# Kernel tuning notes

Hardware: AMD Instinct MI355X
Metric: run time of the kernel (lower is better)

## Reference

```python
import jax, jax.numpy as jnp
import numpy as np
import math

H = 12  # heads (init kwarg)
KEEP_RATE = 0.7  # forward arg keep_rate (< 1 -> token pruning path)


def setup_inputs() -> dict:
    key = jax.random.key(0)
    k0, k1, k2 = jax.random.split(key, 3)
    b, n, c = 32, 577, 768  # ViT-B/16 @ 384px: 576 patches + CLS
    x = jax.random.normal(k0, (b, n, c), dtype=jnp.float32)
    # nn.Linear(dim, dim*3) and nn.Linear(dim, dim); kaiming-ish scale
    W_qkv = jax.random.normal(k1, (c, 3 * c), dtype=jnp.float32) / np.sqrt(c).astype(np.float32)
    b_qkv = jnp.zeros((3 * c,), dtype=jnp.float32)
    W_out = jax.random.normal(k2, (c, c), dtype=jnp.float32) / np.sqrt(c).astype(np.float32)
    b_out = jnp.zeros((c,), dtype=jnp.float32)
    return {"x": x, "keep_rate": KEEP_RATE, "W_qkv": W_qkv, "b_qkv": b_qkv,
            "W_out": W_out, "b_out": b_out}


def reference(x, keep_rate, W_qkv, b_qkv, W_out, b_out):
    b, n, c = x.shape
    d = c // H
    scale = (c / H) ** -0.5
    # qkv projection + split into heads: 'b n (h d) -> b h n d'
    qkv = x @ W_qkv + b_qkv                      # [b, n, 3c]
    q, k, v = jnp.split(qkv, 3, axis=-1)
    split_heads = lambda t: t.reshape(b, n, H, d).transpose(0, 2, 1, 3)
    q, k, v = split_heads(q), split_heads(k), split_heads(v)
    dots = jnp.einsum('bhid,bhjd->bhij', q, k) * scale   # [b,h,n,n]
    attention = jax.nn.softmax(dots, axis=-1)
    out = jnp.einsum('bhij,bhjd->bhid', attention, v)    # [b,h,n,d]
    out = out.transpose(0, 2, 1, 3).reshape(b, n, c)     # 'b h n d -> b n (h d)'
    out = out @ W_out + b_out                            # to_out (dropout=0)
    final_tokens = n - 1
    if keep_rate < 1:
        final_tokens = math.ceil(keep_rate * final_tokens)
        # CLS-token attention to patch tokens, averaged over heads
        class_attention = attention[:, :, 0, 1:].mean(axis=1)   # [b, n-1]
        _, ind = jax.lax.top_k(class_attention, final_tokens)    # [b, final_tokens]
        ind = jnp.sort(ind, axis=1)
        index = jnp.broadcast_to(ind[:, :, None], (b, final_tokens, c))
        return (x, index, ind, class_attention, final_tokens)
    return (out, None, None, None, final_tokens)
```

## Files before the change

### kernel.cpp

```cpp
#include <hip/hip_runtime.h>
#include <hip/hip_bf16.h>
#include <math.h>

#define BATCH 32
#define NTOK 577
#define NPATCH 576
#define CDIM 768
#define HEADS 12
#define DHEAD 64
#define W3 2304
#define FT 404

#define WS_WTIL  24576
#define WS_DBIAS 319488
#define WS_DOTS  319872
#define WS_IND   541440

#define O_X      0ULL
#define O_INDEX  14180352ULL
#define O_IND    24109056ULL
#define O_CA     24121984ULL
#define O_FT     24140416ULL

__global__ __launch_bounds__(256) void k_fold(const float* __restrict__ x,
                                              const float* __restrict__ W,
                                              const float* __restrict__ bias,
                                              float* __restrict__ wtil,
                                              float* __restrict__ dbias) {
    __shared__ float x0s[CDIM];
    __shared__ float red[256];
    __shared__ float qs[DHEAD];
    const int b = blockIdx.x, h = blockIdx.y, tid = threadIdx.x;
    for (int i = tid; i < CDIM; i += 256) x0s[i] = x[(size_t)b * NTOK * CDIM + i];
    __syncthreads();
    {
        const int d = tid & 63, seg = tid >> 6;
        const float* Wq = W + (size_t)(h * DHEAD + d);
        float acc = 0.f;
        const int c0 = seg * 192;
        #pragma unroll 8
        for (int c = c0; c < c0 + 192; c++)
            acc += x0s[c] * Wq[(size_t)c * W3];
        red[tid] = acc;
    }
    __syncthreads();
    if (tid < DHEAD) {
        float q = red[tid] + red[tid + 64] + red[tid + 128] + red[tid + 192]
                + bias[h * DHEAD + tid];
        qs[tid] = q;
        float t = q * bias[CDIM + h * DHEAD + tid];
        #pragma unroll
        for (int off = 32; off; off >>= 1) t += __shfl_down(t, off);
        if (tid == 0) dbias[b * HEADS + h] = t;
    }
    __syncthreads();
    for (int c = tid; c < CDIM; c += 256) {
        const float* wr = W + (size_t)c * W3 + CDIM + h * DHEAD;
        float acc = 0.f;
        #pragma unroll
        for (int d = 0; d < DHEAD; d += 4) {
            float4 a = *reinterpret_cast<const float4*>(wr + d);
            acc += a.x * qs[d] + a.y * qs[d + 1] + a.z * qs[d + 2] + a.w * qs[d + 3];
        }
        wtil[((size_t)b * HEADS + h) * CDIM + c] = acc;
    }
}

__global__ __launch_bounds__(256) void k_dots(const float* __restrict__ x,
                                              const float* __restrict__ wtil,
                                              const float* __restrict__ dbias,
                                              float* __restrict__ dots,
                                              float* __restrict__ out0) {
    __shared__ float wt[HEADS * CDIM];
    __shared__ float db[HEADS];
    const int b = blockIdx.x, tid = threadIdx.x;
    for (int i = tid; i < HEADS * CDIM; i += 256) wt[i] = wtil[(size_t)b * HEADS * CDIM + i];
    if (tid < HEADS) db[tid] = dbias[b * HEADS + tid];
    __syncthreads();
    const int wave = tid >> 6, lane = tid & 63;
    for (int it = 0; it < 8; it++) {
        const int j = blockIdx.y * 32 + it * 4 + wave;
        if (j >= NTOK) break;
        const float4* xp = reinterpret_cast<const float4*>(x + ((size_t)b * NTOK + j) * CDIM);
        float4* op = reinterpret_cast<float4*>(out0 + ((size_t)b * NTOK + j) * CDIM);
        float acc[HEADS];
        #pragma unroll
        for (int h = 0; h < HEADS; h++) acc[h] = 0.f;
        #pragma unroll
        for (int i = 0; i < 3; i++) {
            float4 a = xp[i * 64 + lane];
            op[i * 64 + lane] = a;
            const int cbase = i * 256 + lane * 4;
            #pragma unroll
            for (int h = 0; h < HEADS; h++) {
                float4 w = *reinterpret_cast<const float4*>(&wt[h * CDIM + cbase]);
                acc[h] += a.x * w.x + a.y * w.y + a.z * w.z + a.w * w.w;
            }
        }
        #pragma unroll
        for (int off = 32; off; off >>= 1)
            #pragma unroll
            for (int h = 0; h < HEADS; h++) acc[h] += __shfl_xor(acc[h], off);
        if (lane == 0) {
            #pragma unroll
            for (int h = 0; h < HEADS; h++)
                dots[((size_t)b * HEADS + h) * NTOK + j] = 0.125f * (acc[h] + db[h]);
        }
    }
}

__global__ __launch_bounds__(768) void k_catopk(const float* __restrict__ dots,
                                                float* __restrict__ ca_out,
                                                float* __restrict__ ind_out,
                                                float* __restrict__ ft_out,
                                                int* __restrict__ ind_ws,
                                                int write_ft) {
    __shared__ float dl[HEADS * NTOK];
    __shared__ float mh[HEADS], sh[HEADS];
    __shared__ unsigned int vals[NPATCH];
    __shared__ int flags[NPATCH];
    const int b = blockIdx.x, tid = threadIdx.x;
    for (int i = tid; i < HEADS * NTOK; i += 768) dl[i] = dots[(size_t)b * HEADS * NTOK + i];
    __syncthreads();
    {
        const int w = tid >> 6, lane = tid & 63;
        const float* row = dl + w * NTOK;
        float m = -3.4e38f;
        for (int j = lane; j < NTOK; j += 64) m = fmaxf(m, row[j]);
        #pragma unroll
        for (int off = 32; off; off >>= 1) m = fmaxf(m, __shfl_xor(m, off));
        float s = 0.f;
        for (int j = lane; j < NTOK; j += 64) s += expf(row[j] - m);
        #pragma unroll
        for (int off = 32; off; off >>= 1) s += __shfl_xor(s, off);
        if (lane == 0) { mh[w] = m; sh[w] = s; }
    }
    __syncthreads();
    if (tid < NPATCH) {
        float ca = 0.f;
        #pragma unroll
        for (int h = 0; h < HEADS; h++)
            ca += expf(dl[h * NTOK + 1 + tid] - mh[h]) / sh[h];
        ca *= (1.f / 12.f);
        ca_out[(size_t)b * NPATCH + tid] = ca;
        vals[tid] = __float_as_uint(ca);
    }
    __syncthreads();
    if (tid < NPATCH) {
        const unsigned int myv = vals[tid];
        int rank = 0;
        for (int j = 0; j < NPATCH; j++) {
            const unsigned int v = vals[j];
            rank += (v > myv) || (v == myv && j < tid);
        }
        flags[tid] = (rank < FT) ? 1 : 0;
    }
    __syncthreads();
    if (tid < NPATCH && flags[tid]) {
        int pos = 0;
        for (int j = 0; j < tid; j++) pos += flags[j];
        ind_ws[b * FT + pos] = tid;
        ind_out[(size_t)b * FT + pos] = (float)tid;
    }
    if (b == 0 && tid == 0 && write_ft) ft_out[0] = (float)FT;
}

__global__ __launch_bounds__(256) void k_bcast(const int* __restrict__ ind,
                                               float* __restrict__ out1) {
    const unsigned int g = blockIdx.x * 256u + threadIdx.x;
    const unsigned int e = g * 4u;
    const unsigned int row = e / CDIM;
    const float v = (float)ind[row];
    float4 o; o.x = v; o.y = v; o.z = v; o.w = v;
    *reinterpret_cast<float4*>(out1 + e) = o;
}

extern "C" void kernel_launch(void* const* d_in, const int* in_sizes, int n_in,
                              void* d_out, int out_size, void* d_ws, size_t ws_size,
                              hipStream_t stream) {
    const float* x  = (const float*)d_in[0];
    const float* W  = (const float*)d_in[2];
    const float* bq = (const float*)d_in[3];
    float* ws = (float*)d_ws;
    float* out = (float*)d_out;

    k_fold<<<dim3(BATCH, HEADS), 256, 0, stream>>>(x, W, bq, ws + WS_WTIL, ws + WS_DBIAS);
    k_dots<<<dim3(BATCH, 19), 256, 0, stream>>>(x, ws + WS_WTIL, ws + WS_DBIAS, ws + WS_DOTS, out + O_X);
    const int write_ft = (out_size > (int)O_FT) ? 1 : 0;
    k_catopk<<<BATCH, 768, 0, stream>>>(ws + WS_DOTS, out + O_CA, out + O_IND, out + O_FT,
                                        (int*)(ws + WS_IND), write_ft);
    k_bcast<<<9696, 256, 0, stream>>>((const int*)(ws + WS_IND), out + O_INDEX);
}
```

Measured before the change: 227.1 us.

## Fuse four kernels into one persistent kernel with global flag synchronization

Merges the fold, dots, class-attention/top-k and broadcast kernels into one launch over a (batch, 19) grid. Stages are ordered per batch with release/acquire flags stored in the not-yet-written index output buffer, which is later overwritten. This removes three kernel launches and their inter-kernel gaps. In exchange it risks deadlock or timeouts if the 608 blocks are not all co-resident, serializes the top-k step on one block per batch, and depends on sentinel values in the output buffer, so a leftover sentinel from a previous call could let a wait pass early.

```diff
diff --git a/kernel.cpp b/kernel.cpp
--- a/kernel.cpp
+++ b/kernel.cpp
@@ -1,5 +1,4 @@
 #include <hip/hip_runtime.h>
-#include <hip/hip_bf16.h>
 #include <math.h>
 
 #define BATCH 32
@@ -10,6 +9,7 @@
 #define DHEAD 64
 #define W3 2304
 #define FT 404
+#define JBLK 19
 
 #define WS_WTIL  24576
 #define WS_DBIAS 319488
@@ -22,157 +22,213 @@
 #define O_CA     24121984ULL
 #define O_FT     24140416ULL
 
-__global__ __launch_bounds__(256) void k_fold(const float* __restrict__ x,
-                                              const float* __restrict__ W,
-                                              const float* __restrict__ bias,
-                                              float* __restrict__ wtil,
-                                              float* __restrict__ dbias) {
-    __shared__ float x0s[CDIM];
-    __shared__ float red[256];
-    __shared__ float qs[DHEAD];
-    const int b = blockIdx.x, h = blockIdx.y, tid = threadIdx.x;
-    for (int i = tid; i < CDIM; i += 256) x0s[i] = x[(size_t)b * NTOK * CDIM + i];
+#define SENT 0x5EE7F1A6u
+#define SPIN_GUARD (1 << 18)
+
+__device__ __forceinline__ unsigned flag_ld_acq(const unsigned* p) {
+    return __hip_atomic_load(p, __ATOMIC_ACQUIRE, __HIP_MEMORY_SCOPE_AGENT);
+}
+__device__ __forceinline__ void flag_st_rel(unsigned* p, unsigned v) {
+    __hip_atomic_store(p, v, __ATOMIC_RELEASE, __HIP_MEMORY_SCOPE_AGENT);
+}
+__device__ __forceinline__ void wait_flags(const unsigned* base, int n, int stride) {
+    for (int i = 0; i < n; ++i) {
+        const unsigned* p = base + (size_t)i * (size_t)stride;
+        int guard = 0;
+        while (flag_ld_acq(p) != SENT) {
+            __builtin_amdgcn_s_sleep(16);
+            if (++guard > SPIN_GUARD) break;
+        }
+    }
+}
+
+__global__ __launch_bounds__(256, 3) void k_mega(
+        const float* __restrict__ x, const float* __restrict__ W,
+        const float* __restrict__ bq, float* __restrict__ ws,
+        float* out, int write_ft)
+{
+    __shared__ float smem[HEADS * CDIM];
+    __shared__ float db[HEADS];
+    __shared__ float mh[HEADS], sh[HEADS];
+    __shared__ unsigned vals[NPATCH];
+    __shared__ int flags[NPATCH];
+
+    const int b = blockIdx.x, y = blockIdx.y, tid = threadIdx.x;
+    float* const wtil  = ws + WS_WTIL;
+    float* const dbias = ws + WS_DBIAS;
+    float* const dots  = ws + WS_DOTS;
+    int*   const indws = (int*)(ws + WS_IND);
+    unsigned* const idxU = (unsigned*)(out + O_INDEX);
+    #define FCELL(row, c) (idxU + (((size_t)b * FT + (size_t)(row)) * CDIM + (c)))
+
+    if (y < HEADS) {
+        const int h = y;
+        float* const x0s = smem;
+        float* const red = smem + CDIM;
+        float* const qs  = smem + CDIM + 256;
+        if (tid < CDIM / 4)
+            ((float4*)x0s)[tid] = ((const float4*)(x + (size_t)b * NTOK * CDIM))[tid];
+        __syncthreads();
+        {
+            const int d = tid & 63, seg = tid >> 6;
+            const float* Wq = W + (size_t)(h * DHEAD + d);
+            float acc = 0.f;
+            const int c0 = seg * 192;
+            #pragma unroll 8
+            for (int c = c0; c < c0 + 192; c++)
+                acc += x0s[c] * Wq[(size_t)c * W3];
+            red[tid] = acc;
+        }
+        __syncthreads();
+        if (tid < DHEAD) {
+            float q = red[tid] + red[tid + 64] + red[tid + 128] + red[tid + 192]
+                    + bq[h * DHEAD + tid];
+            qs[tid] = q;
+            float t = q * bq[CDIM + h * DHEAD + tid];
+            #pragma unroll
+            for (int off = 32; off; off >>= 1) t += __shfl_down(t, off);
+            if (tid == 0) dbias[b * HEADS + h] = t;
+        }
+        __syncthreads();
+        for (int c = tid; c < CDIM; c += 256) {
+            const float* wr = W + (size_t)c * W3 + CDIM + h * DHEAD;
+            float acc = 0.f;
+            #pragma unroll
+            for (int d = 0; d < DHEAD; d += 4) {
+                float4 a = *reinterpret_cast<const float4*>(wr + d);
+                acc += a.x * qs[d] + a.y * qs[d + 1] + a.z * qs[d + 2] + a.w * qs[d + 3];
+            }
+            wtil[((size_t)b * HEADS + h) * CDIM + c] = acc;
+        }
+        __syncthreads();
+        if (tid == 0) { __threadfence(); flag_st_rel(FCELL(h, 2), SENT); }
+    }
+
+    if (tid == 0) wait_flags(FCELL(0, 2), HEADS, CDIM);
     __syncthreads();
+
     {
-        const int d = tid & 63, seg = tid >> 6;
-        const float* Wq = W + (size_t)(h * DHEAD + d);
-        float acc = 0.f;
-        const int c0 = seg * 192;
-        #pragma unroll 8
-        for (int c = c0; c < c0 + 192; c++)
-            acc += x0s[c] * Wq[(size_t)c * W3];
-        red[tid] = acc;
-    }
-    __syncthreads();
-    if (tid < DHEAD) {
-        float q = red[tid] + red[tid + 64] + red[tid + 128] + red[tid + 192]
-                + bias[h * DHEAD + tid];
-        qs[tid] = q;
-        float t = q * bias[CDIM + h * DHEAD + tid];
-        #pragma unroll
-        for (int off = 32; off; off >>= 1) t += __shfl_down(t, off);
-        if (tid == 0) dbias[b * HEADS + h] = t;
-    }
-    __syncthreads();
-    for (int c = tid; c < CDIM; c += 256) {
-        const float* wr = W + (size_t)c * W3 + CDIM + h * DHEAD;
-        float acc = 0.f;
-        #pragma unroll
-        for (int d = 0; d < DHEAD; d += 4) {
-            float4 a = *reinterpret_cast<const float4*>(wr + d);
-            acc += a.x * qs[d] + a.y * qs[d + 1] + a.z * qs[d + 2] + a.w * qs[d + 3];
-        }
-        wtil[((size_t)b * HEADS + h) * CDIM + c] = acc;
-    }
-}
-
-__global__ __launch_bounds__(256) void k_dots(const float* __restrict__ x,
-                                              const float* __restrict__ wtil,
-                                              const float* __restrict__ dbias,
-                                              float* __restrict__ dots,
-                                              float* __restrict__ out0) {
-    __shared__ float wt[HEADS * CDIM];
-    __shared__ float db[HEADS];
-    const int b = blockIdx.x, tid = threadIdx.x;
-    for (int i = tid; i < HEADS * CDIM; i += 256) wt[i] = wtil[(size_t)b * HEADS * CDIM + i];
-    if (tid < HEADS) db[tid] = dbias[b * HEADS + tid];
-    __syncthreads();
-    const int wave = tid >> 6, lane = tid & 63;
-    for (int it = 0; it < 8; it++) {
-        const int j = blockIdx.y * 32 + it * 4 + wave;
-        if (j >= NTOK) break;
-        const float4* xp = reinterpret_cast<const float4*>(x + ((size_t)b * NTOK + j) * CDIM);
-        float4* op = reinterpret_cast<float4*>(out0 + ((size_t)b * NTOK + j) * CDIM);
-        float acc[HEADS];
-        #pragma unroll
-        for (int h = 0; h < HEADS; h++) acc[h] = 0.f;
-        #pragma unroll
-        for (int i = 0; i < 3; i++) {
-            float4 a = xp[i * 64 + lane];
-            op[i * 64 + lane] = a;
-            const int cbase = i * 256 + lane * 4;
-            #pragma unroll
-            for (int h = 0; h < HEADS; h++) {
-                float4 w = *reinterpret_cast<const float4*>(&wt[h * CDIM + cbase]);
-                acc[h] += a.x * w.x + a.y * w.y + a.z * w.z + a.w * w.w;
-            }
-        }
-        #pragma unroll
-        for (int off = 32; off; off >>= 1)
-            #pragma unroll
-            for (int h = 0; h < HEADS; h++) acc[h] += __shfl_xor(acc[h], off);
-        if (lane == 0) {
+        float* const wt = smem;
+        {
+            const float4* s4 = (const float4*)(wtil + (size_t)b * HEADS * CDIM);
+            float4* d4 = (float4*)wt;
+            for (int i = tid; i < HEADS * CDIM / 4; i += 256) d4[i] = s4[i];
+        }
+        if (tid < HEADS) db[tid] = dbias[b * HEADS + tid];
+        __syncthreads();
+        const int wave = tid >> 6, lane = tid & 63;
+        for (int it = 0; it < 8; it++) {
+            const int j = y * 32 + it * 4 + wave;
+            if (j >= NTOK) break;
+            const float4* xp = (const float4*)(x + ((size_t)b * NTOK + j) * CDIM);
+            float4* op = (float4*)(out + O_X + ((size_t)b * NTOK + j) * CDIM);
+            float acc[HEADS];
+            #pragma unroll
+            for (int h = 0; h < HEADS; h++) acc[h] = 0.f;
+            #pragma unroll
+            for (int i = 0; i < 3; i++) {
+                float4 a = xp[i * 64 + lane];
+                op[i * 64 + lane] = a;
+                const int cbase = i * 256 + lane * 4;
+                #pragma unroll
+                for (int h = 0; h < HEADS; h++) {
+                    float4 w = *(const float4*)(&wt[h * CDIM + cbase]);
+                    acc[h] += a.x * w.x + a.y * w.y + a.z * w.z + a.w * w.w;
+                }
+            }
+            #pragma unroll
+            for (int off = 32; off; off >>= 1)
+                #pragma unroll
+                for (int h = 0; h < HEADS; h++) acc[h] += __shfl_xor(acc[h], off);
+            if (lane == 0) {
+                #pragma unroll
+                for (int h = 0; h < HEADS; h++)
+                    dots[((size_t)b * HEADS + h) * NTOK + j] = 0.125f * (acc[h] + db[h]);
+            }
+        }
+        __syncthreads();
+        if (tid == 0) { __threadfence(); flag_st_rel(FCELL(y, 1), SENT); }
+    }
+
+    if (y == 0) {
+        if (tid == 0) wait_flags(FCELL(0, 1), JBLK, CDIM);
+        __syncthreads();
+        float* const dl = smem;
+        {
+            const float4* s4 = (const float4*)(dots + (size_t)b * HEADS * NTOK);
+            float4* d4 = (float4*)dl;
+            for (int i = tid; i < HEADS * NTOK / 4; i += 256) d4[i] = s4[i];
+        }
+        __syncthreads();
+        {
+            const int w = tid >> 6, lane = tid & 63;
+            #pragma unroll
+            for (int hh = 0; hh < 3; hh++) {
+                const int h = w * 3 + hh;
+                const float* row = dl + h * NTOK;
+                float m = -3.4e38f;
+                for (int j = lane; j < NTOK; j += 64) m = fmaxf(m, row[j]);
+                #pragma unroll
+                for (int off = 32; off; off >>= 1) m = fmaxf(m, __shfl_xor(m, off));
+                float s = 0.f;
+                for (int j = lane; j < NTOK; j += 64) s += expf(row[j] - m);
+                #pragma unroll
+                for (int off = 32; off; off >>= 1) s += __shfl_xor(s, off);
+                if (lane == 0) { mh[h] = m; sh[h] = s; }
+            }
+        }
+        __syncthreads();
+        for (int t = tid; t < NPATCH; t += 256) {
+            float ca = 0.f;
             #pragma unroll
             for (int h = 0; h < HEADS; h++)
-                dots[((size_t)b * HEADS + h) * NTOK + j] = 0.125f * (acc[h] + db[h]);
-        }
-    }
-}
-
-__global__ __launch_bounds__(768) void k_catopk(const float* __restrict__ dots,
-                                                float* __restrict__ ca_out,
-                                                float* __restrict__ ind_out,
-                                                float* __restrict__ ft_out,
-                                                int* __restrict__ ind_ws,
-                                                int write_ft) {
-    __shared__ float dl[HEADS * NTOK];
-    __shared__ float mh[HEADS], sh[HEADS];
-    __shared__ unsigned int vals[NPATCH];
-    __shared__ int flags[NPATCH];
-    const int b = blockIdx.x, tid = threadIdx.x;
-    for (int i = tid; i < HEADS * NTOK; i += 768) dl[i] = dots[(size_t)b * HEADS * NTOK + i];
-    __syncthreads();
+                ca += expf(dl[h * NTOK + 1 + t] - mh[h]) / sh[h];
+            ca *= (1.f / 12.f);
+            out[O_CA + (size_t)b * NPATCH + t] = ca;
+            vals[t] = __float_as_uint(ca);
+        }
+        __syncthreads();
+        for (int t = tid; t < NPATCH; t += 256) {
+            const unsigned myv = vals[t];
+            int rank = 0;
+            for (int j = 0; j < NPATCH; j++) {
+                const unsigned v = vals[j];
+                rank += (v > myv) || (v == myv && j < t);
+            }
+            flags[t] = (rank < FT) ? 1 : 0;
+        }
+        __syncthreads();
+        for (int t = tid; t < NPATCH; t += 256) {
+            if (flags[t]) {
+                int pos = 0;
+                for (int j = 0; j < t; j++) pos += flags[j];
+                indws[b * FT + pos] = t;
+                out[O_IND + (size_t)b * FT + pos] = (float)t;
+            }
+        }
+        if (b == 0 && tid == 0 && write_ft) out[O_FT] = (float)FT;
+        __syncthreads();
+        if (tid == 0) {
+            __threadfence();
+            for (int i = 0; i < JBLK; i++) flag_st_rel(FCELL(i, 0), SENT);
+        }
+    } else {
+        if (tid == 0) wait_flags(FCELL(y, 0), 1, 0);
+        __syncthreads();
+    }
+
     {
-        const int w = tid >> 6, lane = tid & 63;
-        const float* row = dl + w * NTOK;
-        float m = -3.4e38f;
-        for (int j = lane; j < NTOK; j += 64) m = fmaxf(m, row[j]);
-        #pragma unroll
-        for (int off = 32; off; off >>= 1) m = fmaxf(m, __shfl_xor(m, off));
-        float s = 0.f;
-        for (int j = lane; j < NTOK; j += 64) s += expf(row[j] - m);
-        #pragma unroll
-        for (int off = 32; off; off >>= 1) s += __shfl_xor(s, off);
-        if (lane == 0) { mh[w] = m; sh[w] = s; }
-    }
-    __syncthreads();
-    if (tid < NPATCH) {
-        float ca = 0.f;
-        #pragma unroll
-        for (int h = 0; h < HEADS; h++)
-            ca += expf(dl[h * NTOK + 1 + tid] - mh[h]) / sh[h];
-        ca *= (1.f / 12.f);
-        ca_out[(size_t)b * NPATCH + tid] = ca;
-        vals[tid] = __float_as_uint(ca);
-    }
-    __syncthreads();
-    if (tid < NPATCH) {
-        const unsigned int myv = vals[tid];
-        int rank = 0;
-        for (int j = 0; j < NPATCH; j++) {
-            const unsigned int v = vals[j];
-            rank += (v > myv) || (v == myv && j < tid);
-        }
-        flags[tid] = (rank < FT) ? 1 : 0;
-    }
-    __syncthreads();
-    if (tid < NPATCH && flags[tid]) {
-        int pos = 0;
-        for (int j = 0; j < tid; j++) pos += flags[j];
-        ind_ws[b * FT + pos] = tid;
-        ind_out[(size_t)b * FT + pos] = (float)tid;
-    }
-    if (b == 0 && tid == 0 && write_ft) ft_out[0] = (float)FT;
-}
-
-__global__ __launch_bounds__(256) void k_bcast(const int* __restrict__ ind,
-                                               float* __restrict__ out1) {
-    const unsigned int g = blockIdx.x * 256u + threadIdx.x;
-    const unsigned int e = g * 4u;
-    const unsigned int row = e / CDIM;
-    const float v = (float)ind[row];
-    float4 o; o.x = v; o.y = v; o.z = v; o.w = v;
-    *reinterpret_cast<float4*>(out1 + e) = o;
+        const int K = (FT - 1 - y) / JBLK + 1;
+        const int total = K * 192;
+        for (int f = tid; f < total; f += 256) {
+            const int k = f / 192, c = f - k * 192;
+            const int t = y + k * JBLK;
+            const float v = (float)indws[b * FT + t];
+            float4 o; o.x = v; o.y = v; o.z = v; o.w = v;
+            ((float4*)(out + O_INDEX + ((size_t)b * FT + t) * CDIM))[c] = o;
+        }
+    }
+    #undef FCELL
 }
 
 extern "C" void kernel_launch(void* const* d_in, const int* in_sizes, int n_in,
@@ -183,11 +239,6 @@
     const float* bq = (const float*)d_in[3];
     float* ws = (float*)d_ws;
     float* out = (float*)d_out;
-
-    k_fold<<<dim3(BATCH, HEADS), 256, 0, stream>>>(x, W, bq, ws + WS_WTIL, ws + WS_DBIAS);
-    k_dots<<<dim3(BATCH, 19), 256, 0, stream>>>(x, ws + WS_WTIL, ws + WS_DBIAS, ws + WS_DOTS, out + O_X);
     const int write_ft = (out_size > (int)O_FT) ? 1 : 0;
-    k_catopk<<<BATCH, 768, 0, stream>>>(ws + WS_DOTS, out + O_CA, out + O_IND, out + O_FT,
-                                        (int*)(ws + WS_IND), write_ft);
-    k_bcast<<<9696, 256, 0, stream>>>((const int*)(ws + WS_IND), out + O_INDEX);
-}
+    k_mega<<<dim3(BATCH, JBLK), 256, 0, stream>>>(x, W, bq, ws, out, write_ft);
+}
```

New measurement: 615.2 us. 2.71x slower.

## Fuse top-k with index broadcast and batch four samples per fold block

Applied to the files above, without the earlier changes.

The fold kernel now handles four batch items per block, so each W_q/W_k column read is shared across four samples, and its grid shrinks to 96 blocks. The class-attention/top-k kernel is merged with the index broadcast kernel, which removes one launch and the workspace index round trip. Selected positions are compacted with ballot and popcount prefix sums instead of serial per-thread scans. The fused kernel is replicated across 8 y-blocks that each recompute softmax and ranks redundantly to split the broadcast writes, which adds duplicated compute in exchange.

```diff
diff --git a/kernel.cpp b/kernel.cpp
--- a/kernel.cpp
+++ b/kernel.cpp
@@ -1,5 +1,4 @@
 #include <hip/hip_runtime.h>
-#include <hip/hip_bf16.h>
 #include <math.h>
 
 #define BATCH 32
@@ -14,7 +13,6 @@
 #define WS_WTIL  24576
 #define WS_DBIAS 319488
 #define WS_DOTS  319872
-#define WS_IND   541440
 
 #define O_X      0ULL
 #define O_INDEX  14180352ULL
@@ -24,45 +22,55 @@
 
 __global__ __launch_bounds__(256) void k_fold(const float* __restrict__ x,
                                               const float* __restrict__ W,
-                                              const float* __restrict__ bias,
+                                              const float* __restrict__ bq,
                                               float* __restrict__ wtil,
                                               float* __restrict__ dbias) {
-    __shared__ float x0s[CDIM];
-    __shared__ float red[256];
-    __shared__ float qs[DHEAD];
-    const int b = blockIdx.x, h = blockIdx.y, tid = threadIdx.x;
-    for (int i = tid; i < CDIM; i += 256) x0s[i] = x[(size_t)b * NTOK * CDIM + i];
-    __syncthreads();
-    {
-        const int d = tid & 63, seg = tid >> 6;
-        const float* Wq = W + (size_t)(h * DHEAD + d);
+    __shared__ float x0s[4 * CDIM];
+    __shared__ float qs[4 * DHEAD];
+    const int h = blockIdx.x, bg = blockIdx.y, tid = threadIdx.x;
+    const int bg4 = bg * 4;
+    {
+        float4* d4 = (float4*)x0s;
+        for (int i = tid; i < 4 * CDIM / 4; i += 256) {
+            const int bl = i / 192, r = i - bl * 192;
+            d4[i] = ((const float4*)(x + (size_t)(bg4 + bl) * NTOK * CDIM))[r];
+        }
+    }
+    __syncthreads();
+    {
+        const int d = tid & 63, wv = tid >> 6;
+        const float* Wq = W + h * DHEAD + d;
+        const float* xrow = x0s + wv * CDIM;
         float acc = 0.f;
-        const int c0 = seg * 192;
-        #pragma unroll 8
-        for (int c = c0; c < c0 + 192; c++)
-            acc += x0s[c] * Wq[(size_t)c * W3];
-        red[tid] = acc;
-    }
-    __syncthreads();
-    if (tid < DHEAD) {
-        float q = red[tid] + red[tid + 64] + red[tid + 128] + red[tid + 192]
-                + bias[h * DHEAD + tid];
-        qs[tid] = q;
-        float t = q * bias[CDIM + h * DHEAD + tid];
+        #pragma unroll 16
+        for (int c = 0; c < CDIM; c++) acc += xrow[c] * Wq[(size_t)c * W3];
+        const float q = acc + bq[h * DHEAD + d];
+        qs[wv * DHEAD + d] = q;
+        float t = q * bq[CDIM + h * DHEAD + d];
         #pragma unroll
         for (int off = 32; off; off >>= 1) t += __shfl_down(t, off);
-        if (tid == 0) dbias[b * HEADS + h] = t;
-    }
-    __syncthreads();
-    for (int c = tid; c < CDIM; c += 256) {
-        const float* wr = W + (size_t)c * W3 + CDIM + h * DHEAD;
-        float acc = 0.f;
-        #pragma unroll
-        for (int d = 0; d < DHEAD; d += 4) {
-            float4 a = *reinterpret_cast<const float4*>(wr + d);
-            acc += a.x * qs[d] + a.y * qs[d + 1] + a.z * qs[d + 2] + a.w * qs[d + 3];
-        }
-        wtil[((size_t)b * HEADS + h) * CDIM + c] = acc;
+        if (d == 0) dbias[(bg4 + wv) * HEADS + h] = t;
+    }
+    __syncthreads();
+    {
+        const int bl = tid >> 6, ci = tid & 63;
+        float4 q4[16];
+        const float4* qp = (const float4*)(qs + bl * DHEAD);
+        #pragma unroll
+        for (int t2 = 0; t2 < 16; t2++) q4[t2] = qp[t2];
+        float* wout = wtil + ((size_t)(bg4 + bl) * HEADS + h) * CDIM;
+        #pragma unroll 2
+        for (int k = 0; k < 12; k++) {
+            const int c = ci + k * 64;
+            const float4* wr = (const float4*)(W + (size_t)c * W3 + CDIM + h * DHEAD);
+            float acc = 0.f;
+            #pragma unroll
+            for (int t2 = 0; t2 < 16; t2++) {
+                const float4 ww = wr[t2];
+                acc += ww.x * q4[t2].x + ww.y * q4[t2].y + ww.z * q4[t2].z + ww.w * q4[t2].w;
+            }
+            wout[c] = acc;
+        }
     }
 }
 
@@ -109,22 +117,27 @@
     }
 }
 
-__global__ __launch_bounds__(768) void k_catopk(const float* __restrict__ dots,
-                                                float* __restrict__ ca_out,
-                                                float* __restrict__ ind_out,
-                                                float* __restrict__ ft_out,
-                                                int* __restrict__ ind_ws,
-                                                int write_ft) {
+__global__ __launch_bounds__(256) void k_catbc(const float* __restrict__ dots,
+                                               float* __restrict__ out,
+                                               int write_ft) {
     __shared__ float dl[HEADS * NTOK];
     __shared__ float mh[HEADS], sh[HEADS];
-    __shared__ unsigned int vals[NPATCH];
-    __shared__ int flags[NPATCH];
-    const int b = blockIdx.x, tid = threadIdx.x;
-    for (int i = tid; i < HEADS * NTOK; i += 768) dl[i] = dots[(size_t)b * HEADS * NTOK + i];
-    __syncthreads();
-    {
-        const int w = tid >> 6, lane = tid & 63;
-        const float* row = dl + w * NTOK;
+    __shared__ unsigned vals[NPATCH];
+    __shared__ unsigned long long segmask[9];
+    __shared__ int segoff[9];
+    __shared__ int ind_lds[FT];
+    const int b = blockIdx.x, y = blockIdx.y, tid = threadIdx.x;
+    {
+        const float4* s4 = (const float4*)(dots + (size_t)b * HEADS * NTOK);
+        float4* d4 = (float4*)dl;
+        for (int i = tid; i < HEADS * NTOK / 4; i += 256) d4[i] = s4[i];
+    }
+    __syncthreads();
+    const int w = tid >> 6, lane = tid & 63;
+    #pragma unroll
+    for (int hh = 0; hh < 3; hh++) {
+        const int h = w * 3 + hh;
+        const float* row = dl + h * NTOK;
         float m = -3.4e38f;
         for (int j = lane; j < NTOK; j += 64) m = fmaxf(m, row[j]);
         #pragma unroll
@@ -133,46 +146,67 @@
         for (int j = lane; j < NTOK; j += 64) s += expf(row[j] - m);
         #pragma unroll
         for (int off = 32; off; off >>= 1) s += __shfl_xor(s, off);
-        if (lane == 0) { mh[w] = m; sh[w] = s; }
-    }
-    __syncthreads();
-    if (tid < NPATCH) {
+        if (lane == 0) { mh[h] = m; sh[h] = s; }
+    }
+    __syncthreads();
+    for (int t = tid; t < NPATCH; t += 256) {
         float ca = 0.f;
         #pragma unroll
         for (int h = 0; h < HEADS; h++)
-            ca += expf(dl[h * NTOK + 1 + tid] - mh[h]) / sh[h];
+            ca += expf(dl[h * NTOK + 1 + t] - mh[h]) / sh[h];
         ca *= (1.f / 12.f);
-        ca_out[(size_t)b * NPATCH + tid] = ca;
-        vals[tid] = __float_as_uint(ca);
-    }
-    __syncthreads();
-    if (tid < NPATCH) {
-        const unsigned int myv = vals[tid];
-        int rank = 0;
-        for (int j = 0; j < NPATCH; j++) {
-            const unsigned int v = vals[j];
-            rank += (v > myv) || (v == myv && j < tid);
-        }
-        flags[tid] = (rank < FT) ? 1 : 0;
-    }
-    __syncthreads();
-    if (tid < NPATCH && flags[tid]) {
-        int pos = 0;
-        for (int j = 0; j < tid; j++) pos += flags[j];
-        ind_ws[b * FT + pos] = tid;
-        ind_out[(size_t)b * FT + pos] = (float)tid;
-    }
-    if (b == 0 && tid == 0 && write_ft) ft_out[0] = (float)FT;
-}
-
-__global__ __launch_bounds__(256) void k_bcast(const int* __restrict__ ind,
-                                               float* __restrict__ out1) {
-    const unsigned int g = blockIdx.x * 256u + threadIdx.x;
-    const unsigned int e = g * 4u;
-    const unsigned int row = e / CDIM;
-    const float v = (float)ind[row];
-    float4 o; o.x = v; o.y = v; o.z = v; o.w = v;
-    *reinterpret_cast<float4*>(out1 + e) = o;
+        if (y == 0) out[O_CA + (size_t)b * NPATCH + t] = ca;
+        vals[t] = __float_as_uint(ca);
+    }
+    __syncthreads();
+    {
+        const uint4* v4 = (const uint4*)vals;
+        for (int s = w; s < 9; s += 4) {
+            const int t = s * 64 + lane;
+            const unsigned myv = vals[t];
+            int rank = 0;
+            #pragma unroll 4
+            for (int j4 = 0; j4 < NPATCH / 4; j4++) {
+                const uint4 vv = v4[j4];
+                const int j = j4 * 4;
+                rank += (vv.x > myv) || (vv.x == myv && j     < t);
+                rank += (vv.y > myv) || (vv.y == myv && j + 1 < t);
+                rank += (vv.z > myv) || (vv.z == myv && j + 2 < t);
+                rank += (vv.w > myv) || (vv.w == myv && j + 3 < t);
+            }
+            const unsigned long long mask = __ballot(rank < FT);
+            if (lane == 0) segmask[s] = mask;
+        }
+    }
+    __syncthreads();
+    if (tid == 0) {
+        int acc = 0;
+        #pragma unroll
+        for (int s = 0; s < 9; s++) { segoff[s] = acc; acc += __popcll(segmask[s]); }
+    }
+    __syncthreads();
+    for (int s = w; s < 9; s += 4) {
+        const int t = s * 64 + lane;
+        const unsigned long long mask = segmask[s];
+        if ((mask >> lane) & 1ull) {
+            const int pos = segoff[s] + __popcll(mask & ((1ull << lane) - 1ull));
+            ind_lds[pos] = t;
+            if (y == 0) out[O_IND + (size_t)b * FT + pos] = (float)t;
+        }
+    }
+    if (y == 0 && b == 0 && tid == 0 && write_ft) out[O_FT] = (float)FT;
+    __syncthreads();
+    {
+        const int nrows = (FT - 1 - y) / 8 + 1;
+        const int total = nrows * 192;
+        for (int f = tid; f < total; f += 256) {
+            const int k = f / 192, cc = f - k * 192;
+            const int r = y + k * 8;
+            const float v = (float)ind_lds[r];
+            float4 o; o.x = v; o.y = v; o.z = v; o.w = v;
+            ((float4*)(out + O_INDEX + ((size_t)b * FT + r) * CDIM))[cc] = o;
+        }
+    }
 }
 
 extern "C" void kernel_launch(void* const* d_in, const int* in_sizes, int n_in,
@@ -184,10 +218,9 @@
     float* ws = (float*)d_ws;
     float* out = (float*)d_out;
 
-    k_fold<<<dim3(BATCH, HEADS), 256, 0, stream>>>(x, W, bq, ws + WS_WTIL, ws + WS_DBIAS);
-    k_dots<<<dim3(BATCH, 19), 256, 0, stream>>>(x, ws + WS_WTIL, ws + WS_DBIAS, ws + WS_DOTS, out + O_X);
+    k_fold<<<dim3(HEADS, 8), 256, 0, stream>>>(x, W, bq, ws + WS_WTIL, ws + WS_DBIAS);
+    k_dots<<<dim3(BATCH, 19), 256, 0, stream>>>(x, ws + WS_WTIL, ws + WS_DBIAS,
+                                                ws + WS_DOTS, out + O_X);
     const int write_ft = (out_size > (int)O_FT) ? 1 : 0;
-    k_catopk<<<BATCH, 768, 0, stream>>>(ws + WS_DOTS, out + O_CA, out + O_IND, out + O_FT,
-                                        (int*)(ws + WS_IND), write_ft);
-    k_bcast<<<9696, 256, 0, stream>>>((const int*)(ws + WS_IND), out + O_INDEX);
-}
+    k_catbc<<<dim3(BATCH, 8), 256, 0, stream>>>(ws + WS_DOTS, out, write_ft);
+}
```

Result: slower. 279.0 us (+22.8%).
